# Optimization experiments

Measured on AMD Instinct MI355X. Metric: run time of the kernel, lower is better.

Reference implementation:

```python
import jax, jax.numpy as jnp
import numpy as np

B, N, S = 8, 8192, 1024
K = 16          # max_degree
HIDDEN = 192    # hidden_dim, divisible by 2*ndim -> no padding in sincos embed
NDIM = 3
MAX_WAVELENGTH = 10000.0


def sincos_embed(coords, dim, ndim):
    # Continuous sin/cos embedding: dim//ndim channels per coordinate,
    # half sin / half cos, geometric frequencies (UPT-style).
    dpw = dim // ndim                          # dims per coordinate (even)
    ar = jnp.arange(0, dpw, 2, dtype=coords.dtype)
    omega = 1.0 / (MAX_WAVELENGTH ** (ar / dpw))   # (dpw/2,)
    out = coords[..., None] * omega            # (..., ndim, dpw/2)
    emb = jnp.concatenate([jnp.sin(out), jnp.cos(out)], axis=-1)  # (..., ndim, dpw)
    return emb.reshape(*coords.shape[:-1], dim)


def knn_gather(x, sidx, k):
    # x: (B,N,ndim), sidx: (B,S) -> (B,S,k,ndim) coords of k nearest neighbors.
    # Equivalent to the original dense NxN dists[sidx] + argsort[:, :k],
    # but only computes the S rows that are used and uses top_k.
    def per_sample(sx, si):
        sp = sx[si]                                            # (S, ndim)
        d = jnp.sum((sp[:, None, :] - sx[None, :, :]) ** 2, -1)  # (S, N)
        _, nbr = jax.lax.top_k(-d, k)                          # k smallest dists
        return sx[nbr]                                         # (S, k, ndim)
    return jax.vmap(per_sample)(x, sidx)


def setup_inputs() -> dict:
    key = jax.random.key(0)
    ks = jax.random.split(key, 6)
    scale = 0.02
    return {
        "input_points": jax.random.normal(ks[0], (B, N, NDIM), dtype=jnp.float32),
        "supernode_idxs": jax.random.randint(ks[1], (B, S), 0, N),
        "w_in": jax.random.normal(ks[2], (NDIM, HIDDEN), dtype=jnp.float32) * scale,
        "b_in": jnp.zeros((HIDDEN,), dtype=jnp.float32),
        "w1": jax.random.normal(ks[3], (HIDDEN, HIDDEN), dtype=jnp.float32) * scale,
        "b1": jnp.zeros((HIDDEN,), dtype=jnp.float32),
        "w2": jax.random.normal(ks[4], (HIDDEN, HIDDEN), dtype=jnp.float32) * scale,
        "b2": jnp.zeros((HIDDEN,), dtype=jnp.float32),
    }


def reference(input_points, supernode_idxs, w_in, b_in, w1, b1, w2, b2):
    nbr = knn_gather(input_points, supernode_idxs, K)      # (B,S,K,3)
    # input projection + continuous sincos positional embedding
    h = nbr @ w_in + b_in + sincos_embed(nbr, HIDDEN, NDIM)  # (B,S,K,H)
    # message net: Dense -> gelu -> Dense
    h = jax.nn.gelu(h @ w1 + b1)
    h = h @ w2 + b2
    # mean-pool over neighbors per supernode
    return jnp.mean(h, axis=-2)                            # (B,S,H)
```

## Files before the change

kernel.cpp:

```cpp
#include <hip/hip_runtime.h>
#include <stdint.h>

#define NB   8
#define NPTS 8192
#define NS   1024
#define NK   16
#define NH   192
#define KP1  224
#define HROW 236
#define QTR  2048

typedef float    f32x4 __attribute__((ext_vector_type(4)));
typedef short    s16x8 __attribute__((ext_vector_type(8)));
typedef uint32_t u32;
typedef unsigned long long u64;

constexpr float OMEGA[32] = {
  1.0f, 0.74989420933245585f, 0.56234132519034907f, 0.42169650342858223f,
  0.31622776601683794f, 0.23713737056616552f, 0.17782794100389229f, 0.13335214321633237f,
  0.1f, 0.074989420933245585f, 0.056234132519034907f, 0.042169650342858223f,
  0.031622776601683794f, 0.023713737056616552f, 0.017782794100389229f, 0.013335214321633237f,
  0.01f, 0.0074989420933245585f, 0.0056234132519034907f, 0.0042169650342858223f,
  0.0031622776601683794f, 0.0023713737056616552f, 0.0017782794100389229f, 0.0013335214321633237f,
  0.001f, 0.00074989420933245585f, 0.00056234132519034907f, 0.00042169650342858223f,
  0.00031622776601683794f, 0.00023713737056616552f, 0.00017782794100389229f, 0.00013335214321633237f };

__device__ __forceinline__ uint16_t f2bf(float f) {
  u32 u = __float_as_uint(f);
  return (uint16_t)((u + 0x7FFFu + ((u >> 16) & 1u)) >> 16);
}
__device__ __forceinline__ u32 pk2bf(float f0, float f1) {
  return ((__float_as_uint(f0) + 0x8000u) >> 16) |
         ((__float_as_uint(f1) + 0x8000u) & 0xFFFF0000u);
}

__global__ void __launch_bounds__(64) prep_weights(
    const float* __restrict__ w_in, const float* __restrict__ b_in,
    const float* __restrict__ w1, const float* __restrict__ b1,
    const float* __restrict__ w2,
    uint16_t* __restrict__ wT1e, uint16_t* __restrict__ wT2) {
  const int n = blockIdx.x, t = threadIdx.x;
  float p0 = 0, p1 = 0, p2 = 0, pb = 0;
  #pragma unroll
  for (int kk = 0; kk < 3; ++kk) {
    int c = kk * 64 + t;
    float w1cn = w1[c * NH + n];
    wT1e[n * KP1 + c] = f2bf(w1cn);
    wT2 [n * NH  + c] = f2bf(w2[c * NH + n]);
    p0 = fmaf(w_in[0 * NH + c], w1cn, p0);
    p1 = fmaf(w_in[1 * NH + c], w1cn, p1);
    p2 = fmaf(w_in[2 * NH + c], w1cn, p2);
    pb = fmaf(b_in[c], w1cn, pb);
  }
  #pragma unroll
  for (int off = 32; off; off >>= 1) {
    p0 += __shfl_down(p0, off);
    p1 += __shfl_down(p1, off);
    p2 += __shfl_down(p2, off);
    pb += __shfl_down(pb, off);
  }
  if (t == 0) {
    wT1e[n * KP1 + 192] = f2bf(p0);
    wT1e[n * KP1 + 193] = f2bf(p1);
    wT1e[n * KP1 + 194] = f2bf(p2);
    wT1e[n * KP1 + 195] = f2bf(pb + b1[n]);
  }
  if (t >= 4 && t < 32) wT1e[n * KP1 + 192 + t] = 0;
}

__global__ void __launch_bounds__(512, 8) knn_kernel(const float* __restrict__ pts,
                                                     const int* __restrict__ sidx,
                                                     u64* __restrict__ keys) {
  __shared__ float2 XY[QTR];
  __shared__ float  Zs[QTR];
  const int bid = blockIdx.x;
  const int b = bid >> 7;
  const int chunk = (bid >> 2) & 31;
  const int quarter = bid & 3;
  const int pbase = quarter * QTR;
  const float* pb = pts + ((size_t)b * NPTS + pbase) * 3;
  for (int i = threadIdx.x; i < QTR; i += 512) {
    XY[i] = float2{pb[3 * i], pb[3 * i + 1]};
    Zs[i] = pb[3 * i + 2];
  }
  __syncthreads();
  const int wave = threadIdx.x >> 6, lane = threadIdx.x & 63;
  const int sbase = chunk * 32 + wave * 4;

  float sx[4], sy[4], sz[4], minD[4], Td[4];
  u32 minI[4];
  u64 arr[4], T[4];
  #pragma unroll
  for (int q = 0; q < 4; ++q) {
    int si = sidx[b * NS + sbase + q];
    const float* qp = pts + ((size_t)b * NPTS + si) * 3;
    sx[q] = qp[0]; sy[q] = qp[1]; sz[q] = qp[2];
    minD[q] = __uint_as_float(0x7F800000u);
    minI[q] = 0xFFFFFFFFu;
  }

  {
    float2 xy = XY[lane];
    float  z  = Zs[lane];
    for (int t = 0; t < QTR / 64; ++t) {
      float2 xyc = xy; float zc = z;
      if (t + 1 < QTR / 64) { xy = XY[(t + 1) * 64 + lane]; z = Zs[(t + 1) * 64 + lane]; }
      int lj = t * 64 + lane;
      #pragma unroll
      for (int q = 0; q < 4; ++q) {
        float dx = xyc.x - sx[q], dy = xyc.y - sy[q], dz = zc - sz[q];
        float d = __fadd_rn(__fadd_rn(__fmul_rn(dx, dx), __fmul_rn(dy, dy)),
                            __fmul_rn(dz, dz));
        bool c = d < minD[q];
        minD[q] = c ? d : minD[q];
        minI[q] = c ? (u32)(pbase + lj) : minI[q];
      }
    }
  }

  #pragma unroll
  for (int q = 0; q < 4; ++q) {
    u64 key = ((u64)__float_as_uint(minD[q]) << 32) | minI[q];
    #pragma unroll
    for (int k = 2; k <= 64; k <<= 1) {
      #pragma unroll
      for (int jj = k >> 1; jj > 0; jj >>= 1) {
        u64 p = __shfl_xor(key, jj);
        bool takeMin = (((lane & jj) == 0) == ((lane & k) == 0));
        key = (takeMin == (p < key)) ? p : key;
      }
    }
    arr[q] = (lane < 16) ? key : ~0ull;
    T[q] = __shfl(key, 15);
    Td[q] = __uint_as_float((u32)(T[q] >> 32));
  }

  {
    float2 xy = XY[lane];
    float  z  = Zs[lane];
    for (int t = 0; t < QTR / 64; ++t) {
      float2 xyc = xy; float zc = z;
      if (t + 1 < QTR / 64) { xy = XY[(t + 1) * 64 + lane]; z = Zs[(t + 1) * 64 + lane]; }
      int lj = t * 64 + lane;
      #pragma unroll
      for (int q = 0; q < 4; ++q) {
        float dx = xyc.x - sx[q], dy = xyc.y - sy[q], dz = zc - sz[q];
        float d = __fadd_rn(__fadd_rn(__fmul_rn(dx, dx), __fmul_rn(dy, dy)),
                            __fmul_rn(dz, dz));
        u64 ball = __ballot(d <= Td[q] && (u32)(pbase + lj) != minI[q]);
        if (ball) {
          u64 key = ((u64)__float_as_uint(d) << 32) | (u32)(pbase + lj);
          do {
            int src = __builtin_ctzll(ball);
            ball &= ball - 1;
            u64 k2 = __shfl(key, src);
            if (k2 < T[q]) {
              int r = __popcll(__ballot(arr[q] < k2));
              u64 up = __shfl_up(arr[q], 1);
              if (lane == r) arr[q] = k2;
              else if (lane > r && lane < 16) arr[q] = up;
              T[q] = __shfl(arr[q], 15);
              Td[q] = __uint_as_float((u32)(T[q] >> 32));
            }
          } while (ball);
        }
      }
    }
  }
  #pragma unroll
  for (int q = 0; q < 4; ++q)
    if (lane < 16)
      keys[((size_t)(b * NS + sbase + q)) * 64 + quarter * 16 + lane] = arr[q];
}

__device__ __forceinline__ float h0ch(int c, float c0, float c1, float c2) {
  if (c >= 196) return 0.0f;
  if (c == 195) return 1.0f;
  if (c == 192) return c0;
  if (c == 193) return c1;
  if (c == 194) return c2;
  int dd = c >> 6, i = c & 63, m = i & 31;
  float coord = (dd == 0) ? c0 : ((dd == 1) ? c1 : c2);
  float arg = coord * OMEGA[m];
  return (i < 32) ? __sinf(arg) : __cosf(arg);
}

__device__ __forceinline__ float gelu_f(float x) {
  float v = -1.5957691216057308f * __fmaf_rn(0.044715f * x, x * x, x);
  return x * __builtin_amdgcn_rcpf(1.0f + __expf(v));
}

__global__ void __launch_bounds__(256) mlp_kernel(
    const float* __restrict__ pts, const u64* __restrict__ keys,
    const float* __restrict__ b2v,
    const uint16_t* __restrict__ wT1e, const uint16_t* __restrict__ wT2,
    float* __restrict__ out) {
  __shared__ uint16_t hbuf[128 * HROW];
  __shared__ int nbrL[128];
  const int g = blockIdx.x, tid = threadIdx.x;
  const int wave = tid >> 6, lane = tid & 63;
  const int lrow = lane & 15, lg = lane >> 4;

  #pragma unroll
  for (int ii = 0; ii < 2; ++ii) {
    int q = ii * 4 + wave;
    int list = lane >> 4, pos = lane & 15;
    int rpos = (list & 1) ? (15 - pos) : pos;
    u64 key = keys[((size_t)g * 8 + q) * 64 + list * 16 + rpos];
    #pragma unroll
    for (int jj = 16; jj > 0; jj >>= 1) {
      u64 p = __shfl_xor(key, jj);
      bool takeMin = (((lane & jj) == 0) == ((lane & 32) == 0));
      key = (takeMin == (p < key)) ? p : key;
    }
    #pragma unroll
    for (int jj = 32; jj > 0; jj >>= 1) {
      u64 p = __shfl_xor(key, jj);
      bool takeMin = ((lane & jj) == 0);
      key = (takeMin == (p < key)) ? p : key;
    }
    if (lane < 16) nbrL[q * 16 + lane] = (int)(u32)key;
  }
  __syncthreads();

  {
    int r = tid >> 1, half = tid & 1;
    int grow = g * 128 + r;
    int b = grow >> 14;
    int pidx = nbrL[r];
    const float* pp = pts + ((size_t)b * NPTS + pidx) * 3;
    float c0 = pp[0], c1 = pp[1], c2 = pp[2];
    if (half == 0) {
      #pragma unroll
      for (int jj = 0; jj < 28; ++jj) {
        const int c = jj * 4;
        uint2 pk;
        pk.x = pk2bf(h0ch(c,     c0, c1, c2), h0ch(c + 1, c0, c1, c2));
        pk.y = pk2bf(h0ch(c + 2, c0, c1, c2), h0ch(c + 3, c0, c1, c2));
        *(uint2*)(hbuf + r * HROW + c) = pk;
      }
    } else {
      #pragma unroll
      for (int jj = 0; jj < 28; ++jj) {
        const int c = 112 + jj * 4;
        uint2 pk;
        pk.x = pk2bf(h0ch(c,     c0, c1, c2), h0ch(c + 1, c0, c1, c2));
        pk.y = pk2bf(h0ch(c + 2, c0, c1, c2), h0ch(c + 3, c0, c1, c2));
        *(uint2*)(hbuf + r * HROW + c) = pk;
      }
    }
  }
  __syncthreads();

  f32x4 acc1[3][8] = {};
  {
    const uint16_t* wbase = wT1e + (size_t)(wave * 48 + lrow) * KP1 + lg * 8;
    uint4 anx[3];
    #pragma unroll
    for (int nt = 0; nt < 3; ++nt) anx[nt] = *(const uint4*)(wbase + nt * 16 * KP1);
    #pragma unroll
    for (int kk = 0; kk < 7; ++kk) {
      uint4 acur[3];
      #pragma unroll
      for (int nt = 0; nt < 3; ++nt) acur[nt] = anx[nt];
      if (kk < 6) {
        #pragma unroll
        for (int nt = 0; nt < 3; ++nt)
          anx[nt] = *(const uint4*)(wbase + nt * 16 * KP1 + (kk + 1) * 32);
      }
      s16x8 bm[8];
      #pragma unroll
      for (int mt = 0; mt < 8; ++mt)
        bm[mt] = __builtin_bit_cast(s16x8,
                   *(const uint4*)(hbuf + (mt * 16 + lrow) * HROW + kk * 32 + lg * 8));
      #pragma unroll
      for (int nt = 0; nt < 3; ++nt)
        #pragma unroll
        for (int mt = 0; mt < 8; ++mt)
          acc1[nt][mt] = __builtin_amdgcn_mfma_f32_16x16x32_bf16(
              __builtin_bit_cast(s16x8, acur[nt]), bm[mt], acc1[nt][mt], 0, 0, 0);
    }
  }
  __syncthreads();

  {
    #pragma unroll
    for (int nt = 0; nt < 3; ++nt) {
      #pragma unroll
      for (int mt = 0; mt < 8; ++mt) {
        uint2 pk;
        pk.x = pk2bf(gelu_f(acc1[nt][mt][0]), gelu_f(acc1[nt][mt][1]));
        pk.y = pk2bf(gelu_f(acc1[nt][mt][2]), gelu_f(acc1[nt][mt][3]));
        *(uint2*)(hbuf + (mt * 16 + lrow) * HROW + wave * 48 + nt * 16 + lg * 4) = pk;
      }
    }
  }
  __syncthreads();

  f32x4 acc2[8][3] = {};
  {
    const uint16_t* w2base = wT2 + (size_t)(wave * 48 + lrow) * NH + lg * 8;
    uint4 bnx[3];
    #pragma unroll
    for (int nt = 0; nt < 3; ++nt) bnx[nt] = *(const uint4*)(w2base + nt * 16 * NH);
    #pragma unroll
    for (int kk = 0; kk < 6; ++kk) {
      uint4 bcur[3];
      #pragma unroll
      for (int nt = 0; nt < 3; ++nt) bcur[nt] = bnx[nt];
      if (kk < 5) {
        #pragma unroll
        for (int nt = 0; nt < 3; ++nt)
          bnx[nt] = *(const uint4*)(w2base + nt * 16 * NH + (kk + 1) * 32);
      }
      s16x8 am[8];
      #pragma unroll
      for (int mt = 0; mt < 8; ++mt)
        am[mt] = __builtin_bit_cast(s16x8,
                   *(const uint4*)(hbuf + (mt * 16 + lrow) * HROW + kk * 32 + lg * 8));
      #pragma unroll
      for (int mt = 0; mt < 8; ++mt)
        #pragma unroll
        for (int nt = 0; nt < 3; ++nt)
          acc2[mt][nt] = __builtin_amdgcn_mfma_f32_16x16x32_bf16(
              am[mt], __builtin_bit_cast(s16x8, bcur[nt]), acc2[mt][nt], 0, 0, 0);
    }
  }

  {
    #pragma unroll
    for (int mt = 0; mt < 8; ++mt) {
      #pragma unroll
      for (int nt = 0; nt < 3; ++nt) {
        float ssum = acc2[mt][nt][0] + acc2[mt][nt][1] + acc2[mt][nt][2] + acc2[mt][nt][3];
        ssum += __shfl_xor(ssum, 16);
        ssum += __shfl_xor(ssum, 32);
        if (lane < 16) {
          int col = wave * 48 + nt * 16 + lrow;
          out[(size_t)(g * 8 + mt) * NH + col] = ssum * 0.0625f + b2v[col];
        }
      }
    }
  }
}

extern "C" void kernel_launch(void* const* d_in, const int* in_sizes, int n_in,
                              void* d_out, int out_size, void* d_ws, size_t ws_size,
                              hipStream_t stream) {
  (void)in_sizes; (void)n_in; (void)out_size; (void)ws_size;
  const float* pts  = (const float*)d_in[0];
  const int*   sidx = (const int*)d_in[1];
  const float* w_in = (const float*)d_in[2];
  const float* b_in = (const float*)d_in[3];
  const float* w1   = (const float*)d_in[4];
  const float* b1   = (const float*)d_in[5];
  const float* w2   = (const float*)d_in[6];
  const float* b2   = (const float*)d_in[7];
  float* out = (float*)d_out;

  u64* keys = (u64*)d_ws;
  uint16_t* wT1e = (uint16_t*)((char*)d_ws + (size_t)NB * NS * 64 * 8);
  uint16_t* wT2  = wT1e + NH * KP1;

  hipLaunchKernelGGL(prep_weights, dim3(NH), dim3(64), 0, stream,
                     w_in, b_in, w1, b1, w2, wT1e, wT2);

  hipLaunchKernelGGL(knn_kernel, dim3(NB * 128), dim3(512), 0, stream,
                     pts, sidx, keys);

  hipLaunchKernelGGL(mlp_kernel, dim3(NB * NS / 8), dim3(256), 0, stream,
                     pts, keys, b2, wT1e, wT2, out);
}
```

Before: 90.56 us.

## Shrink MLP LDS row, build coord/bias K-tile in registers, deepen weight prefetch

The hidden buffer row stride drops from 236 to 196 elements. The last K-slice of the first GEMM (raw coordinates plus a constant 1 for the bias) is now built in registers from a small coordinate table instead of being stored in LDS. Weight loads are double-buffered two K-steps ahead, occupancy is hinted with launch_bounds(256,3), and the software prefetch in the kNN distance loops is removed. Smaller LDS use is meant to allow more resident blocks, at the cost of extra registers for the deeper prefetch and possible LDS bank conflicts from the new row stride.

```diff
diff --git a/kernel.cpp b/kernel.cpp
--- a/kernel.cpp
+++ b/kernel.cpp
@@ -7,7 +7,7 @@
 #define NK   16
 #define NH   192
 #define KP1  224
-#define HROW 236
+#define HROW 196
 #define QTR  2048
 
 typedef float    f32x4 __attribute__((ext_vector_type(4)));
@@ -99,22 +99,18 @@
     minI[q] = 0xFFFFFFFFu;
   }
 
-  {
-    float2 xy = XY[lane];
-    float  z  = Zs[lane];
-    for (int t = 0; t < QTR / 64; ++t) {
-      float2 xyc = xy; float zc = z;
-      if (t + 1 < QTR / 64) { xy = XY[(t + 1) * 64 + lane]; z = Zs[(t + 1) * 64 + lane]; }
-      int lj = t * 64 + lane;
-      #pragma unroll
-      for (int q = 0; q < 4; ++q) {
-        float dx = xyc.x - sx[q], dy = xyc.y - sy[q], dz = zc - sz[q];
-        float d = __fadd_rn(__fadd_rn(__fmul_rn(dx, dx), __fmul_rn(dy, dy)),
-                            __fmul_rn(dz, dz));
-        bool c = d < minD[q];
-        minD[q] = c ? d : minD[q];
-        minI[q] = c ? (u32)(pbase + lj) : minI[q];
-      }
+  for (int t = 0; t < QTR / 64; ++t) {
+    int lj = t * 64 + lane;
+    float2 xy = XY[lj];
+    float z = Zs[lj];
+    #pragma unroll
+    for (int q = 0; q < 4; ++q) {
+      float dx = xy.x - sx[q], dy = xy.y - sy[q], dz = z - sz[q];
+      float d = __fadd_rn(__fadd_rn(__fmul_rn(dx, dx), __fmul_rn(dy, dy)),
+                          __fmul_rn(dz, dz));
+      bool c = d < minD[q];
+      minD[q] = c ? d : minD[q];
+      minI[q] = c ? (u32)(pbase + lj) : minI[q];
     }
   }
 
@@ -135,35 +131,31 @@
     Td[q] = __uint_as_float((u32)(T[q] >> 32));
   }
 
-  {
-    float2 xy = XY[lane];
-    float  z  = Zs[lane];
-    for (int t = 0; t < QTR / 64; ++t) {
-      float2 xyc = xy; float zc = z;
-      if (t + 1 < QTR / 64) { xy = XY[(t + 1) * 64 + lane]; z = Zs[(t + 1) * 64 + lane]; }
-      int lj = t * 64 + lane;
-      #pragma unroll
-      for (int q = 0; q < 4; ++q) {
-        float dx = xyc.x - sx[q], dy = xyc.y - sy[q], dz = zc - sz[q];
-        float d = __fadd_rn(__fadd_rn(__fmul_rn(dx, dx), __fmul_rn(dy, dy)),
-                            __fmul_rn(dz, dz));
-        u64 ball = __ballot(d <= Td[q] && (u32)(pbase + lj) != minI[q]);
-        if (ball) {
-          u64 key = ((u64)__float_as_uint(d) << 32) | (u32)(pbase + lj);
-          do {
-            int src = __builtin_ctzll(ball);
-            ball &= ball - 1;
-            u64 k2 = __shfl(key, src);
-            if (k2 < T[q]) {
-              int r = __popcll(__ballot(arr[q] < k2));
-              u64 up = __shfl_up(arr[q], 1);
-              if (lane == r) arr[q] = k2;
-              else if (lane > r && lane < 16) arr[q] = up;
-              T[q] = __shfl(arr[q], 15);
-              Td[q] = __uint_as_float((u32)(T[q] >> 32));
-            }
-          } while (ball);
-        }
+  for (int t = 0; t < QTR / 64; ++t) {
+    int lj = t * 64 + lane;
+    float2 xy = XY[lj];
+    float z = Zs[lj];
+    #pragma unroll
+    for (int q = 0; q < 4; ++q) {
+      float dx = xy.x - sx[q], dy = xy.y - sy[q], dz = z - sz[q];
+      float d = __fadd_rn(__fadd_rn(__fmul_rn(dx, dx), __fmul_rn(dy, dy)),
+                          __fmul_rn(dz, dz));
+      u64 ball = __ballot(d <= Td[q] && (u32)(pbase + lj) != minI[q]);
+      if (ball) {
+        u64 key = ((u64)__float_as_uint(d) << 32) | (u32)(pbase + lj);
+        do {
+          int src = __builtin_ctzll(ball);
+          ball &= ball - 1;
+          u64 k2 = __shfl(key, src);
+          if (k2 < T[q]) {
+            int r = __popcll(__ballot(arr[q] < k2));
+            u64 up = __shfl_up(arr[q], 1);
+            if (lane == r) arr[q] = k2;
+            else if (lane > r && lane < 16) arr[q] = up;
+            T[q] = __shfl(arr[q], 15);
+            Td[q] = __uint_as_float((u32)(T[q] >> 32));
+          }
+        } while (ball);
       }
     }
   }
@@ -174,11 +166,6 @@
 }
 
 __device__ __forceinline__ float h0ch(int c, float c0, float c1, float c2) {
-  if (c >= 196) return 0.0f;
-  if (c == 195) return 1.0f;
-  if (c == 192) return c0;
-  if (c == 193) return c1;
-  if (c == 194) return c2;
   int dd = c >> 6, i = c & 63, m = i & 31;
   float coord = (dd == 0) ? c0 : ((dd == 1) ? c1 : c2);
   float arg = coord * OMEGA[m];
@@ -190,16 +177,18 @@
   return x * __builtin_amdgcn_rcpf(1.0f + __expf(v));
 }
 
-__global__ void __launch_bounds__(256) mlp_kernel(
+__global__ void __launch_bounds__(256, 3) mlp_kernel(
     const float* __restrict__ pts, const u64* __restrict__ keys,
     const float* __restrict__ b2v,
     const uint16_t* __restrict__ wT1e, const uint16_t* __restrict__ wT2,
     float* __restrict__ out) {
   __shared__ uint16_t hbuf[128 * HROW];
+  __shared__ float crdL[128][3];
   __shared__ int nbrL[128];
   const int g = blockIdx.x, tid = threadIdx.x;
   const int wave = tid >> 6, lane = tid & 63;
   const int lrow = lane & 15, lg = lane >> 4;
+  const int ns = wave;
 
   #pragma unroll
   for (int ii = 0; ii < 2; ++ii) {
@@ -230,23 +219,25 @@
     int pidx = nbrL[r];
     const float* pp = pts + ((size_t)b * NPTS + pidx) * 3;
     float c0 = pp[0], c1 = pp[1], c2 = pp[2];
+    uint16_t* hrow = hbuf + r * HROW;
     if (half == 0) {
-      #pragma unroll
-      for (int jj = 0; jj < 28; ++jj) {
+      crdL[r][0] = c0; crdL[r][1] = c1; crdL[r][2] = c2;
+      #pragma unroll
+      for (int jj = 0; jj < 24; ++jj) {
         const int c = jj * 4;
         uint2 pk;
         pk.x = pk2bf(h0ch(c,     c0, c1, c2), h0ch(c + 1, c0, c1, c2));
         pk.y = pk2bf(h0ch(c + 2, c0, c1, c2), h0ch(c + 3, c0, c1, c2));
-        *(uint2*)(hbuf + r * HROW + c) = pk;
+        *(uint2*)(hrow + c) = pk;
       }
     } else {
       #pragma unroll
-      for (int jj = 0; jj < 28; ++jj) {
-        const int c = 112 + jj * 4;
+      for (int jj = 0; jj < 24; ++jj) {
+        const int c = 96 + jj * 4;
         uint2 pk;
         pk.x = pk2bf(h0ch(c,     c0, c1, c2), h0ch(c + 1, c0, c1, c2));
         pk.y = pk2bf(h0ch(c + 2, c0, c1, c2), h0ch(c + 3, c0, c1, c2));
-        *(uint2*)(hbuf + r * HROW + c) = pk;
+        *(uint2*)(hrow + c) = pk;
       }
     }
   }
@@ -254,25 +245,41 @@
 
   f32x4 acc1[3][8] = {};
   {
-    const uint16_t* wbase = wT1e + (size_t)(wave * 48 + lrow) * KP1 + lg * 8;
-    uint4 anx[3];
-    #pragma unroll
-    for (int nt = 0; nt < 3; ++nt) anx[nt] = *(const uint4*)(wbase + nt * 16 * KP1);
+    const uint16_t* wbase = wT1e + (size_t)(ns * 48 + lrow) * KP1 + lg * 8;
+    uint4 anx[2][3];
+    #pragma unroll
+    for (int nt = 0; nt < 3; ++nt) {
+      anx[0][nt] = *(const uint4*)(wbase + nt * 16 * KP1);
+      anx[1][nt] = *(const uint4*)(wbase + nt * 16 * KP1 + 32);
+    }
     #pragma unroll
     for (int kk = 0; kk < 7; ++kk) {
       uint4 acur[3];
       #pragma unroll
-      for (int nt = 0; nt < 3; ++nt) acur[nt] = anx[nt];
+      for (int nt = 0; nt < 3; ++nt) acur[nt] = anx[kk & 1][nt];
+      if (kk < 5) {
+        #pragma unroll
+        for (int nt = 0; nt < 3; ++nt)
+          anx[kk & 1][nt] = *(const uint4*)(wbase + nt * 16 * KP1 + (kk + 2) * 32);
+      }
+      s16x8 bm[8];
       if (kk < 6) {
         #pragma unroll
-        for (int nt = 0; nt < 3; ++nt)
-          anx[nt] = *(const uint4*)(wbase + nt * 16 * KP1 + (kk + 1) * 32);
-      }
-      s16x8 bm[8];
-      #pragma unroll
-      for (int mt = 0; mt < 8; ++mt)
-        bm[mt] = __builtin_bit_cast(s16x8,
-                   *(const uint4*)(hbuf + (mt * 16 + lrow) * HROW + kk * 32 + lg * 8));
+        for (int mt = 0; mt < 8; ++mt)
+          bm[mt] = __builtin_bit_cast(s16x8,
+                     *(const uint4*)(hbuf + (mt * 16 + lrow) * HROW + kk * 32 + lg * 8));
+      } else {
+        #pragma unroll
+        for (int mt = 0; mt < 8; ++mt) {
+          uint4 t{0, 0, 0, 0};
+          if (lg == 0) {
+            const float* cp = crdL[mt * 16 + lrow];
+            t.x = pk2bf(cp[0], cp[1]);
+            t.y = pk2bf(cp[2], 1.0f);
+          }
+          bm[mt] = __builtin_bit_cast(s16x8, t);
+        }
+      }
       #pragma unroll
       for (int nt = 0; nt < 3; ++nt)
         #pragma unroll
@@ -291,7 +298,7 @@
         uint2 pk;
         pk.x = pk2bf(gelu_f(acc1[nt][mt][0]), gelu_f(acc1[nt][mt][1]));
         pk.y = pk2bf(gelu_f(acc1[nt][mt][2]), gelu_f(acc1[nt][mt][3]));
-        *(uint2*)(hbuf + (mt * 16 + lrow) * HROW + wave * 48 + nt * 16 + lg * 4) = pk;
+        *(uint2*)(hbuf + (mt * 16 + lrow) * HROW + ns * 48 + nt * 16 + lg * 4) = pk;
       }
     }
   }
@@ -299,19 +306,22 @@
 
   f32x4 acc2[8][3] = {};
   {
-    const uint16_t* w2base = wT2 + (size_t)(wave * 48 + lrow) * NH + lg * 8;
-    uint4 bnx[3];
-    #pragma unroll
-    for (int nt = 0; nt < 3; ++nt) bnx[nt] = *(const uint4*)(w2base + nt * 16 * NH);
+    const uint16_t* w2base = wT2 + (size_t)(ns * 48 + lrow) * NH + lg * 8;
+    uint4 bnx[2][3];
+    #pragma unroll
+    for (int nt = 0; nt < 3; ++nt) {
+      bnx[0][nt] = *(const uint4*)(w2base + nt * 16 * NH);
+      bnx[1][nt] = *(const uint4*)(w2base + nt * 16 * NH + 32);
+    }
     #pragma unroll
     for (int kk = 0; kk < 6; ++kk) {
       uint4 bcur[3];
       #pragma unroll
-      for (int nt = 0; nt < 3; ++nt) bcur[nt] = bnx[nt];
-      if (kk < 5) {
+      for (int nt = 0; nt < 3; ++nt) bcur[nt] = bnx[kk & 1][nt];
+      if (kk < 4) {
         #pragma unroll
         for (int nt = 0; nt < 3; ++nt)
-          bnx[nt] = *(const uint4*)(w2base + nt * 16 * NH + (kk + 1) * 32);
+          bnx[kk & 1][nt] = *(const uint4*)(w2base + nt * 16 * NH + (kk + 2) * 32);
       }
       s16x8 am[8];
       #pragma unroll
@@ -336,7 +346,7 @@
         ssum += __shfl_xor(ssum, 16);
         ssum += __shfl_xor(ssum, 32);
         if (lane < 16) {
-          int col = wave * 48 + nt * 16 + lrow;
+          int col = ns * 48 + nt * 16 + lrow;
           out[(size_t)(g * 8 + mt) * NH + col] = ssum * 0.0625f + b2v[col];
         }
       }
```

After: 92.14 us. About the same (+1.7%).
